# Kernel optimization log

Measured on AMD Instinct MI355X. Metric: run time of the kernel, lower is better.

The kernel has to match this reference:

```python
import jax, jax.numpy as jnp
import numpy as np

PATCH = 16
LOSS_WEIGHT = 1.0


def setup_inputs() -> dict:
    key = jax.random.key(0)
    cls_score = jax.random.normal(key, (8, 19, 512, 512), dtype=jnp.float32)
    return {"cls_score": cls_score}


def reference(cls_score):
    # Faithful to NuclearLoss(patch_size=16, use_softmax=True, inverse=False,
    # reduction='mean').
    N, C, H, W = cls_score.shape
    p = PATCH
    ph, pw = H // p, W // p
    logits = jax.nn.softmax(cls_score, axis=1)  # softmax over channel dim
    # patchify: (N,C,H,W) -> (N*L, p*p, C) with L = ph*pw
    x = logits.reshape(N, C, ph, p, pw, p)
    x = jnp.einsum('nchpwq->nhwpqc', x)
    patches = x.reshape(N * ph * pw, p * p, C)  # (B, p^2, C)
    # Original: mats = sqrt(bmm(P^T, P)) elementwise, loss = -sum(trace(mat)).
    # Only the diagonal of P^T P is needed: diag_k = sum_i P[i,k]^2.
    diag = jnp.sum(patches * patches, axis=1)          # (B, C)
    loss = -jnp.sum(jnp.sqrt(diag))
    loss = loss / patches.shape[0]                      # reduction='mean'
    return LOSS_WEIGHT * loss
```

## Files before the change

kernel.cpp:

```cpp
#include <hip/hip_runtime.h>
#include <math.h>


#define NIMG 8
#define CCH  19
#define HH   512
#define WW   512
#define CHST (HH * WW)

__global__ __launch_bounds__(256, 4) void nuclear_loss_kernel(
    const float* __restrict__ in, float* __restrict__ out) {
    __shared__ float psum[4 * CCH];

    const int tid = threadIdx.x;
    const int b   = blockIdx.x;
    const int n    = b >> 8;
    const int rem  = b & 255;
    const int prow = rem >> 3;
    const int creg = rem & 7;
    const int col  = (creg << 6) + (tid & 63);
    const int row0 = (prow << 4) + (tid >> 6);
    const int plocal = (tid & 63) >> 4;

    for (int i = tid; i < 4 * CCH; i += 256) psum[i] = 0.0f;
    __syncthreads();

    float part[CCH];
#pragma unroll
    for (int c = 0; c < CCH; ++c) part[c] = 0.0f;

    const float* base = in + (size_t)n * CCH * CHST + (size_t)row0 * WW + col;

#pragma unroll
    for (int i = 0; i < 4; ++i) {
        const float* p = base + (size_t)(i * 4) * WW;
        float e[CCH];
        float s = 0.0f;
#pragma unroll
        for (int c = 0; c < CCH; ++c) {
            e[c] = __expf(p[(size_t)c * CHST]);
            s += e[c];
        }
        const float inv = 1.0f / s;
#pragma unroll
        for (int c = 0; c < CCH; ++c) {
            const float t = e[c] * inv;
            part[c] = fmaf(t, t, part[c]);
        }
    }

#pragma unroll
    for (int c = 0; c < CCH; ++c) {
        float v = part[c];
        v += __shfl_down(v, 8, 16);
        v += __shfl_down(v, 4, 16);
        v += __shfl_down(v, 2, 16);
        v += __shfl_down(v, 1, 16);
        part[c] = v;
    }

    if ((tid & 15) == 0) {
#pragma unroll
        for (int c = 0; c < CCH; ++c)
            atomicAdd(&psum[plocal * CCH + c], part[c]);
    }
    __syncthreads();

    if (tid < 64) {
        float v = (tid < 4 * CCH) ? sqrtf(psum[tid]) : 0.0f;
        if (tid + 64 < 4 * CCH) v += sqrtf(psum[tid + 64]);
        v += __shfl_down(v, 32, 64);
        v += __shfl_down(v, 16, 64);
        v += __shfl_down(v, 8, 64);
        v += __shfl_down(v, 4, 64);
        v += __shfl_down(v, 2, 64);
        v += __shfl_down(v, 1, 64);
        if (tid == 0) atomicAdd(out, v * (-1.0f / 8192.0f));
    }
}

extern "C" void kernel_launch(void* const* d_in, const int* in_sizes, int n_in,
                              void* d_out, int out_size, void* d_ws, size_t ws_size,
                              hipStream_t stream) {
    const float* in = (const float*)d_in[0];
    float* out = (float*)d_out;
    hipMemsetAsync(out, 0, sizeof(float), stream);
    nuclear_loss_kernel<<<2048, 256, 0, stream>>>(in, out);
}
```

Baseline: 223.0 us.

## Load float4 per thread and issue all channel loads upfront

Each thread now covers one row and four adjacent columns, loading all 19 channels as float4 vectors before any compute instead of four scalar rows in sequence. This puts more loads in flight per thread and cuts instruction count. The division becomes a hardware reciprocal, and the per-channel reduction becomes a cross-row xor shuffle followed by a 4-lane reduce. It costs more registers (76 floats held live), which may lower occupancy under the 256x4 launch bound.

```diff
diff --git a/kernel.cpp b/kernel.cpp
--- a/kernel.cpp
+++ b/kernel.cpp
@@ -12,70 +12,72 @@
     const float* __restrict__ in, float* __restrict__ out) {
     __shared__ float psum[4 * CCH];
 
-    const int tid = threadIdx.x;
-    const int b   = blockIdx.x;
+    const int tid  = threadIdx.x;
+    const int b    = blockIdx.x;
     const int n    = b >> 8;
     const int rem  = b & 255;
     const int prow = rem >> 3;
     const int creg = rem & 7;
-    const int col  = (creg << 6) + (tid & 63);
-    const int row0 = (prow << 4) + (tid >> 6);
-    const int plocal = (tid & 63) >> 4;
+    const int cg   = tid & 15;
+    const int row  = (prow << 4) + (tid >> 4);
+    const int col  = (creg << 6) + (cg << 2);
 
     for (int i = tid; i < 4 * CCH; i += 256) psum[i] = 0.0f;
     __syncthreads();
 
-    float part[CCH];
+    const float* bp = in + (size_t)n * (size_t)(CCH * CHST)
+                         + (size_t)row * WW + col;
+
+    float4 v[CCH];
 #pragma unroll
-    for (int c = 0; c < CCH; ++c) part[c] = 0.0f;
+    for (int c = 0; c < CCH; ++c)
+        v[c] = *reinterpret_cast<const float4*>(bp + (size_t)c * CHST);
 
-    const float* base = in + (size_t)n * CCH * CHST + (size_t)row0 * WW + col;
+    float sx = 0.f, sy = 0.f, sz = 0.f, sw = 0.f;
+#pragma unroll
+    for (int c = 0; c < CCH; ++c) {
+        v[c].x = __expf(v[c].x); sx += v[c].x;
+        v[c].y = __expf(v[c].y); sy += v[c].y;
+        v[c].z = __expf(v[c].z); sz += v[c].z;
+        v[c].w = __expf(v[c].w); sw += v[c].w;
+    }
+    const float ix = __builtin_amdgcn_rcpf(sx);
+    const float iy = __builtin_amdgcn_rcpf(sy);
+    const float iz = __builtin_amdgcn_rcpf(sz);
+    const float iw = __builtin_amdgcn_rcpf(sw);
 
-#pragma unroll
-    for (int i = 0; i < 4; ++i) {
-        const float* p = base + (size_t)(i * 4) * WW;
-        float e[CCH];
-        float s = 0.0f;
-#pragma unroll
-        for (int c = 0; c < CCH; ++c) {
-            e[c] = __expf(p[(size_t)c * CHST]);
-            s += e[c];
-        }
-        const float inv = 1.0f / s;
-#pragma unroll
-        for (int c = 0; c < CCH; ++c) {
-            const float t = e[c] * inv;
-            part[c] = fmaf(t, t, part[c]);
-        }
-    }
+    const int  lane   = tid & 63;
+    const bool lead   = (lane < 16) && ((lane & 3) == 0);
+    const int  plocal = cg >> 2;
 
 #pragma unroll
     for (int c = 0; c < CCH; ++c) {
-        float v = part[c];
-        v += __shfl_down(v, 8, 16);
-        v += __shfl_down(v, 4, 16);
-        v += __shfl_down(v, 2, 16);
-        v += __shfl_down(v, 1, 16);
-        part[c] = v;
-    }
-
-    if ((tid & 15) == 0) {
-#pragma unroll
-        for (int c = 0; c < CCH; ++c)
-            atomicAdd(&psum[plocal * CCH + c], part[c]);
+        const float tx = v[c].x * ix;
+        const float ty = v[c].y * iy;
+        const float tz = v[c].z * iz;
+        const float tw = v[c].w * iw;
+        float x = tx * tx;
+        x = fmaf(ty, ty, x);
+        x = fmaf(tz, tz, x);
+        x = fmaf(tw, tw, x);
+        x += __shfl_xor(x, 16, 64);
+        x += __shfl_xor(x, 32, 64);
+        x += __shfl_down(x, 2, 4);
+        x += __shfl_down(x, 1, 4);
+        if (lead) atomicAdd(&psum[plocal * CCH + c], x);
     }
     __syncthreads();
 
     if (tid < 64) {
-        float v = (tid < 4 * CCH) ? sqrtf(psum[tid]) : 0.0f;
-        if (tid + 64 < 4 * CCH) v += sqrtf(psum[tid + 64]);
-        v += __shfl_down(v, 32, 64);
-        v += __shfl_down(v, 16, 64);
-        v += __shfl_down(v, 8, 64);
-        v += __shfl_down(v, 4, 64);
-        v += __shfl_down(v, 2, 64);
-        v += __shfl_down(v, 1, 64);
-        if (tid == 0) atomicAdd(out, v * (-1.0f / 8192.0f));
+        float v2 = (tid < 4 * CCH) ? sqrtf(psum[tid]) : 0.0f;
+        if (tid + 64 < 4 * CCH) v2 += sqrtf(psum[tid + 64]);
+        v2 += __shfl_down(v2, 32, 64);
+        v2 += __shfl_down(v2, 16, 64);
+        v2 += __shfl_down(v2, 8, 64);
+        v2 += __shfl_down(v2, 4, 64);
+        v2 += __shfl_down(v2, 2, 64);
+        v2 += __shfl_down(v2, 1, 64);
+        if (tid == 0) atomicAdd(out, v2 * (-1.0f / 8192.0f));
     }
 }
 
```

After: 219.8 us. About the same (-1.4%).
